# Kernel optimization log

Hardware: AMD Instinct MI355X
Metric: run time of the kernel (lower is better)

The kernel has to match this reference:

```python
import math
import jax, jax.numpy as jnp
import numpy as np

HEAD_SIZE = 64
DEPTH = 0

def lambda_init_fn(depth):
    depth = depth + 1
    return 0.8 - 0.6 * math.exp(-0.3 * depth)

def setup_inputs() -> dict:
    key = jax.random.key(0)
    ks = jax.random.split(key, 9)
    B, T, C = 4, 4096, 1024
    H2 = 2 * HEAD_SIZE  # 128
    return {
        "x":  jax.random.normal(ks[0], (B, T, C), dtype=jnp.float32),
        "Wq": jax.random.normal(ks[1], (C, H2), dtype=jnp.float32) * (C ** -0.5),
        "Wk": jax.random.normal(ks[2], (C, H2), dtype=jnp.float32) * (C ** -0.5),
        "Wv": jax.random.normal(ks[3], (C, H2), dtype=jnp.float32) * (C ** -0.5),
        "lambda_q1": jax.random.normal(ks[4], (HEAD_SIZE,), dtype=jnp.float32) * 0.1,
        "lambda_q2": jax.random.normal(ks[5], (HEAD_SIZE,), dtype=jnp.float32) * 0.1,
        "lambda_k1": jax.random.normal(ks[6], (HEAD_SIZE,), dtype=jnp.float32) * 0.1,
        "lambda_k2": jax.random.normal(ks[7], (HEAD_SIZE,), dtype=jnp.float32) * 0.1,
    }

def reference(x, Wq, Wk, Wv, lambda_q1, lambda_q2, lambda_k1, lambda_k2):
    B, T, C = x.shape
    q = x @ Wq  # (B,T,2*hs)
    k = x @ Wk
    v = x @ Wv  # (B,T,2*hs)
    q1, q2 = jnp.split(q, 2, axis=-1)
    k1, k2 = jnp.split(k, 2, axis=-1)
    scale = 1.0 / math.sqrt(HEAD_SIZE)
    w1 = jnp.einsum('btd,bsd->bts', q1, k1) * scale  # (B,T,T)
    w2 = jnp.einsum('btd,bsd->bts', q2, k2) * scale
    causal = jnp.tril(jnp.ones((T, T), dtype=bool))
    neg_inf = jnp.float32(-jnp.inf)
    w1 = jnp.where(causal, w1, neg_inf)
    w2 = jnp.where(causal, w2, neg_inf)
    lam1 = jnp.exp(jnp.sum(lambda_q1 * lambda_k1))
    lam2 = jnp.exp(jnp.sum(lambda_q2 * lambda_k2))
    lam = lam1 - lam2 + lambda_init_fn(DEPTH)
    weights = jax.nn.softmax(w1, axis=-1) - lam * jax.nn.softmax(w2, axis=-1)
    out = jnp.einsum('bts,bsd->btd', weights, v)  # (B,T,2*hs)
    return out
```

## Files before the change

### kernel.cpp

```cpp
#include <hip/hip_runtime.h>
#include <hip/hip_bf16.h>

typedef __bf16 bf16x8 __attribute__((ext_vector_type(8)));
typedef float f32x4 __attribute__((ext_vector_type(4)));

#define LAMBDA_INIT 0.3555090675909693f
#define CEXP 0.18033688011112042f

#define K_OFF   ((size_t)16384 * 128)
#define VT_OFF  ((size_t)2 * 16384 * 128)
#define PART_OFF_BYTES ((size_t)12582912)
#define REC_FLOATS 4160

__device__ __forceinline__ unsigned short f2bf(float f) {
    __hip_bfloat16 h = __float2bfloat16(f);
    unsigned short u;
    __builtin_memcpy(&u, &h, 2);
    return u;
}
__device__ __forceinline__ float bf2f(unsigned short u) {
    unsigned int x = ((unsigned int)u) << 16;
    float f;
    __builtin_memcpy(&f, &x, 4);
    return f;
}
__device__ __forceinline__ unsigned int cvt_pk_bf16(float a, float b) {
    unsigned int r;
    asm volatile("v_cvt_pk_bf16_f32 %0, %1, %2" : "=v"(r) : "v"(a), "v"(b));
    return r;
}

__global__ __launch_bounds__(256) void prep_wt(
    const float* __restrict__ Wq, const float* __restrict__ Wk,
    const float* __restrict__ Wv, unsigned short* __restrict__ WT) {
    const int kt = blockIdx.x, nt = blockIdx.y, mat = blockIdx.z;
    const float* W = (mat == 0) ? Wq : (mat == 1) ? Wk : Wv;
    unsigned short* O = WT + (size_t)mat * 128 * 1024;
    __shared__ float tb[64][65];
    const int r = threadIdx.x >> 2, c4 = (threadIdx.x & 3) * 16;
    for (int j = 0; j < 4; ++j) {
        float4 v = *(const float4*)&W[(size_t)(kt * 64 + r) * 128 + nt * 64 + c4 + j * 4];
        tb[r][c4 + j * 4 + 0] = v.x;
        tb[r][c4 + j * 4 + 1] = v.y;
        tb[r][c4 + j * 4 + 2] = v.z;
        tb[r][c4 + j * 4 + 3] = v.w;
    }
    __syncthreads();
    unsigned short tmp[16];
    for (int j = 0; j < 16; ++j) tmp[j] = f2bf(tb[c4 + j][r]);
    *(uint4*)&O[(size_t)(nt * 64 + r) * 1024 + kt * 64 + c4] = *(uint4*)&tmp[0];
    *(uint4*)&O[(size_t)(nt * 64 + r) * 1024 + kt * 64 + c4 + 8] = *(uint4*)&tmp[8];
}

__global__ __launch_bounds__(512) void qkv_fused(
    const float* __restrict__ x, const unsigned short* __restrict__ WT,
    unsigned short* __restrict__ qkv) {
    const int tid = threadIdx.x;
    const int l = tid & 63, w = tid >> 6;
    const int g = l >> 4, i16 = l & 15;
    const int rh = w >> 2, cp = w & 3;
    const int row0 = blockIdx.x * 64;
    const int np = blockIdx.y;
    const unsigned short* Wt = WT + (size_t)np * 192 * 1024;

    __shared__ unsigned short xs[64][72];
    __shared__ unsigned short wt[192][72];

    f32x4 acc[2][3];
    const f32x4 z4 = {0.f, 0.f, 0.f, 0.f};
    for (int rt = 0; rt < 2; ++rt)
        for (int ct = 0; ct < 3; ++ct) acc[rt][ct] = z4;

    const int xrow = tid >> 3, xcol = (tid & 7) * 8;
    const int wn = tid >> 3, wk8 = (tid & 7) * 8;
    const float* xp = &x[(size_t)(row0 + xrow) * 1024 + xcol];
    const unsigned short* wp = &Wt[(size_t)wn * 1024 + wk8];

    float4 ax0, ax1;
    uint4 aw0, aw1, aw2;

#define QI(k0_) do {                                                        \
        ax0 = *(const float4*)&xp[(k0_)];                                   \
        ax1 = *(const float4*)&xp[(k0_) + 4];                               \
        aw0 = *(const uint4*)&wp[(k0_)];                                    \
        aw1 = *(const uint4*)&wp[64 * 1024 + (k0_)];                        \
        aw2 = *(const uint4*)&wp[128 * 1024 + (k0_)];                       \
    } while (0)

#define QS() do {                                                           \
        *(ushort4*)&xs[xrow][xcol]     = make_ushort4(f2bf(ax0.x), f2bf(ax0.y), f2bf(ax0.z), f2bf(ax0.w)); \
        *(ushort4*)&xs[xrow][xcol + 4] = make_ushort4(f2bf(ax1.x), f2bf(ax1.y), f2bf(ax1.z), f2bf(ax1.w)); \
        *(uint4*)&wt[wn +   0][wk8] = aw0;                                  \
        *(uint4*)&wt[wn +  64][wk8] = aw1;                                  \
        *(uint4*)&wt[wn + 128][wk8] = aw2;                                  \
    } while (0)

    QI(0);
    #pragma unroll 1
    for (int k0 = 0; k0 < 1024; k0 += 64) {
        __syncthreads();
        QS();
        if (k0 + 64 < 1024) QI(k0 + 64);
        __syncthreads();
        bf16x8 af[2][2];
        #pragma unroll
        for (int rt = 0; rt < 2; ++rt)
            for (int cc = 0; cc < 2; ++cc)
                af[rt][cc] = *(const bf16x8*)&xs[rh * 32 + rt * 16 + i16][cc * 32 + 8 * g];
        #pragma unroll
        for (int ct = 0; ct < 3; ++ct)
            for (int cc = 0; cc < 2; ++cc) {
                bf16x8 bb = *(const bf16x8*)&wt[cp * 48 + ct * 16 + i16][cc * 32 + 8 * g];
                for (int rt = 0; rt < 2; ++rt)
                    acc[rt][ct] = __builtin_amdgcn_mfma_f32_16x16x32_bf16(af[rt][cc], bb, acc[rt][ct], 0, 0, 0);
            }
    }
#undef QI
#undef QS

    __syncthreads();
    unsigned short(*ts)[200] = (unsigned short(*)[200]) & wt[0][0];
    #pragma unroll
    for (int rt = 0; rt < 2; ++rt)
        for (int ct = 0; ct < 3; ++ct) {
            const float sc = (np == 0 && cp * 48 + ct * 16 < 128) ? CEXP : 1.0f;
            for (int r = 0; r < 4; ++r)
                ts[rh * 32 + rt * 16 + g * 4 + r][cp * 48 + ct * 16 + i16] = f2bf(acc[rt][ct][r] * sc);
        }
    __syncthreads();

    const int bq = row0 >> 12;
    const int s = (row0 >> 6) & 63;
    if (np == 0) {
        {
            unsigned short* outp = qkv + (size_t)row0 * 128;
            #pragma unroll
            for (int it = 0; it < 2; ++it) {
                int tr = it * 32 + (tid >> 4), dv0 = (tid & 15) * 8;
                *(uint4*)&outp[tr * 128 + dv0] = *(const uint4*)&ts[tr][dv0];
            }
        }
        {
            unsigned short* kimg = qkv + K_OFF + ((size_t)(bq * 64 + s) * 2) * 4096;
            int region = tid >> 6, slot = tid & 63;
            int row = (region >> 1) * 16 + (slot & 15);
            int d = 128 + (region & 1) * 32 + (slot >> 4) * 8;
            uint4 vv = *(const uint4*)&ts[row][d];
            *(uint4*)&kimg[(region * 64 + slot) * 8] = vv;
        }
    } else {
        {
            unsigned short* kimg = qkv + K_OFF + ((size_t)(bq * 64 + s) * 2 + 1) * 4096;
            int region = tid >> 6, slot = tid & 63;
            int row = (region >> 1) * 16 + (slot & 15);
            int d = (region & 1) * 32 + (slot >> 4) * 8;
            uint4 vv = *(const uint4*)&ts[row][d];
            *(uint4*)&kimg[(region * 64 + slot) * 8] = vv;
        }
        {
            unsigned short* vimg = qkv + VT_OFF + (size_t)(bq * 64 + s) * 8192;
            #pragma unroll
            for (int it = 0; it < 2; ++it) {
                int lin = it * 512 + tid;
                int region = lin >> 6, slot = lin & 63;
                int dv = 64 + (region >> 1) * 16 + (slot & 15);
                int kv0 = (region & 1) * 32 + (slot >> 4) * 8;
                unsigned short tmp[8];
                #pragma unroll
                for (int e = 0; e < 8; ++e) tmp[e] = ts[kv0 + e][dv];
                *(uint4*)&vimg[(region * 64 + slot) * 8] = *(uint4*)tmp;
            }
        }
    }
}

__global__ __launch_bounds__(256, 3) void diff_attn_pair(
    const unsigned short* __restrict__ q, const unsigned short* __restrict__ kimg,
    const unsigned short* __restrict__ vimg,
    float* __restrict__ part, int ncs) {
    const int bx = blockIdx.x, b = blockIdx.y;
    const int c = blockIdx.z >> 1, branch = blockIdx.z & 1;
    const int bxe = (c & 1) ? (31 - bx) : bx;
    const int t_o = 63 - 2 * bxe, t_e = t_o - 1;
    const int n = t_o + 1;
    const int s_lo = (c * n) >> ncs, smax = ((c + 1) * n) >> ncs;

    if (s_lo >= smax) return;

    const int tid = threadIdx.x;
    const int l = tid & 63, w = tid >> 6;
    const int gq = l >> 4, i16 = l & 15;
    const float NEGINF = -__builtin_inff();

    __shared__ unsigned short ksf[2][4096];
    __shared__ unsigned short psf[2][8192];

    float* recA = part + ((((size_t)(b * 64 + t_e) << ncs) + c) * 2 + branch) * REC_FLOATS;
    float* recB = part + ((((size_t)(b * 64 + t_o) << ncs) + c) * 2 + branch) * REC_FLOATS;
    const bool emptyA = (s_lo > t_e);

    const size_t bbase = (size_t)b * 4096;
    const unsigned short* kimg_b = kimg + (size_t)b * 524288;
    const unsigned short* vimg_b = vimg + (size_t)b * 524288;
    const int tid8 = tid * 8;
    const int l8 = l * 8;
    const f32x4 z4 = {0.f, 0.f, 0.f, 0.f};

    bf16x8 qfA[2], qfB[2];
    #pragma unroll
    for (int cc = 0; cc < 2; ++cc) {
        qfA[cc] = *(const bf16x8*)&q[(bbase + t_e * 64 + w * 16 + i16) * 128 + branch * 64 + cc * 32 + 8 * gq];
        qfB[cc] = *(const bf16x8*)&q[(bbase + t_o * 64 + w * 16 + i16) * 128 + branch * 64 + cc * 32 + 8 * gq];
    }

    float lsumA = 0.f, lsumB = 0.f;
    f32x4 acc[2][4][2];
    for (int qs = 0; qs < 2; ++qs)
        for (int qg = 0; qg < 4; ++qg)
            for (int j = 0; j < 2; ++j) acc[qs][qg][j] = z4;

    int pdst[4];
    #pragma unroll
    for (int cb = 0; cb < 4; ++cb)
        pdst[cb] = ((w * 2 + (cb >> 1)) * 64 + ((cb & 1) * 2 + (gq >> 1)) * 16 + i16) * 8 + (gq & 1) * 4;

    uint4 kr0, kr1;
    bf16x8 vb00, vb01, vb10, vb11;

#define K_ISSUE(s_) do {                                                            \
        const unsigned short* kp = &kimg_b[((size_t)(s_) * 2 + branch) * 4096];     \
        kr0 = *(const uint4*)&kp[tid8];                                             \
        kr1 = *(const uint4*)&kp[tid8 + 2048];                                      \
    } while (0)
#define V_ISSUE(s_) do {                                                            \
        const unsigned short* vp = &vimg_b[(size_t)(s_) * 8192 + w * 2048];         \
        vb00 = *(const bf16x8*)&vp[l8];                                             \
        vb01 = *(const bf16x8*)&vp[512 + l8];                                       \
        vb10 = *(const bf16x8*)&vp[1024 + l8];                                      \
        vb11 = *(const bf16x8*)&vp[1536 + l8];                                      \
    } while (0)

#define PV_CLUSTER(pp_, aPrev_) do {                                                \
        if (aPrev_) {                                                               \
            _Pragma("unroll")                                                       \
            for (int qg = 0; qg < 4; ++qg) {                                        \
                bf16x8 pa0 = *(const bf16x8*)&psf[pp_][(qg * 2 + 0) * 512 + l8];    \
                bf16x8 pa1 = *(const bf16x8*)&psf[pp_][(qg * 2 + 1) * 512 + l8];    \
                acc[0][qg][0] = __builtin_amdgcn_mfma_f32_16x16x32_bf16(pa0, vb00, acc[0][qg][0], 0, 0, 0); \
                acc[0][qg][0] = __builtin_amdgcn_mfma_f32_16x16x32_bf16(pa1, vb01, acc[0][qg][0], 0, 0, 0); \
                acc[0][qg][1] = __builtin_amdgcn_mfma_f32_16x16x32_bf16(pa0, vb10, acc[0][qg][1], 0, 0, 0); \
                acc[0][qg][1] = __builtin_amdgcn_mfma_f32_16x16x32_bf16(pa1, vb11, acc[0][qg][1], 0, 0, 0); \
            }                                                                       \
        }                                                                           \
        _Pragma("unroll")                                                           \
        for (int qg = 0; qg < 4; ++qg) {                                            \
            bf16x8 pa0 = *(const bf16x8*)&psf[pp_][4096 + (qg * 2 + 0) * 512 + l8]; \
            bf16x8 pa1 = *(const bf16x8*)&psf[pp_][4096 + (qg * 2 + 1) * 512 + l8]; \
            acc[1][qg][0] = __builtin_amdgcn_mfma_f32_16x16x32_bf16(pa0, vb00, acc[1][qg][0], 0, 0, 0); \
            acc[1][qg][0] = __builtin_amdgcn_mfma_f32_16x16x32_bf16(pa1, vb01, acc[1][qg][0], 0, 0, 0); \
            acc[1][qg][1] = __builtin_amdgcn_mfma_f32_16x16x32_bf16(pa0, vb10, acc[1][qg][1], 0, 0, 0); \
            acc[1][qg][1] = __builtin_amdgcn_mfma_f32_16x16x32_bf16(pa1, vb11, acc[1][qg][1], 0, 0, 0); \
        }                                                                           \
    } while (0)

    K_ISSUE(s_lo);
    #pragma unroll 1
    for (int s = s_lo; s < smax; ++s) {
        const int kb = s & 1;
        *(uint4*)&ksf[kb][tid8] = kr0;
        *(uint4*)&ksf[kb][tid8 + 2048] = kr1;
        if (s + 1 < smax) K_ISSUE(s + 1);
        __syncthreads();

        __builtin_amdgcn_s_setprio(1);
        if (s > s_lo) PV_CLUSTER((s - 1) & 1, (s - 1) != t_o);
        f32x4 scA[4], scB[4];
        for (int cb = 0; cb < 4; ++cb) { scA[cb] = z4; scB[cb] = z4; }
        #pragma unroll
        for (int cb = 0; cb < 4; ++cb)
            for (int cc = 0; cc < 2; ++cc) {
                bf16x8 kf = *(const bf16x8*)&ksf[kb][((cb * 2 + cc) * 64 + l) * 8];
                scA[cb] = __builtin_amdgcn_mfma_f32_16x16x32_bf16(kf, qfA[cc], scA[cb], 0, 0, 0);
                scB[cb] = __builtin_amdgcn_mfma_f32_16x16x32_bf16(kf, qfB[cc], scB[cb], 0, 0, 0);
            }
        __builtin_amdgcn_s_setprio(0);
        V_ISSUE(s);

        const bool aAct = (s != t_o);
        if (aAct) {
            if (s == t_e) {
                int ql = w * 16 + i16;
                for (int cb = 0; cb < 4; ++cb)
                    for (int r = 0; r < 4; ++r)
                        if (cb * 16 + gq * 4 + r > ql) scA[cb][r] = NEGINF;
            }
            #pragma unroll
            for (int cb = 0; cb < 4; ++cb) {
                float p0 = exp2f(scA[cb][0]);
                float p1 = exp2f(scA[cb][1]);
                float p2 = exp2f(scA[cb][2]);
                float p3 = exp2f(scA[cb][3]);
                lsumA += (p0 + p1) + (p2 + p3);
                uint2 pw;
                pw.x = cvt_pk_bf16(p0, p1);
                pw.y = cvt_pk_bf16(p2, p3);
                *(uint2*)&psf[kb][pdst[cb]] = pw;
            }
        }
        {
            if (s == t_o) {
                int ql = w * 16 + i16;
                for (int cb = 0; cb < 4; ++cb)
                    for (int r = 0; r < 4; ++r)
                        if (cb * 16 + gq * 4 + r > ql) scB[cb][r] = NEGINF;
            }
            #pragma unroll
            for (int cb = 0; cb < 4; ++cb) {
                float p0 = exp2f(scB[cb][0]);
                float p1 = exp2f(scB[cb][1]);
                float p2 = exp2f(scB[cb][2]);
                float p3 = exp2f(scB[cb][3]);
                lsumB += (p0 + p1) + (p2 + p3);
                uint2 pw;
                pw.x = cvt_pk_bf16(p0, p1);
                pw.y = cvt_pk_bf16(p2, p3);
                *(uint2*)&psf[kb][4096 + pdst[cb]] = pw;
            }
        }
    }

    __syncthreads();
    __builtin_amdgcn_s_setprio(1);
    PV_CLUSTER((smax - 1) & 1, (smax - 1) != t_o);
    __builtin_amdgcn_s_setprio(0);
#undef K_ISSUE
#undef V_ISSUE
#undef PV_CLUSTER

    lsumA += __shfl_xor(lsumA, 16);
    lsumA += __shfl_xor(lsumA, 32);
    lsumB += __shfl_xor(lsumB, 16);
    lsumB += __shfl_xor(lsumB, 32);
    if (!emptyA) {
        if (gq == 0) recA[w * 16 + i16] = lsumA;
        unsigned short* OA = (unsigned short*)(recA + 64);
        for (int qg = 0; qg < 4; ++qg)
            for (int j = 0; j < 2; ++j)
                for (int r = 0; r < 4; ++r)
                    OA[(qg * 16 + gq * 4 + r) * 128 + (w * 2 + j) * 16 + i16] = f2bf(acc[0][qg][j][r]);
    }
    {
        if (gq == 0) recB[w * 16 + i16] = lsumB;
        unsigned short* OB = (unsigned short*)(recB + 64);
        for (int qg = 0; qg < 4; ++qg)
            for (int j = 0; j < 2; ++j)
                for (int r = 0; r < 4; ++r)
                    OB[(qg * 16 + gq * 4 + r) * 128 + (w * 2 + j) * 16 + i16] = f2bf(acc[1][qg][j][r]);
    }
}

__global__ __launch_bounds__(256) void diff_combine(
    const float* __restrict__ part,
    const float* __restrict__ lq1, const float* __restrict__ lq2,
    const float* __restrict__ lk1, const float* __restrict__ lk2,
    float* __restrict__ out, int ncs) {
    const int t = blockIdx.x, b = blockIdx.y;
    const int tid = threadIdx.x;
    const int nc = 1 << ncs;
    const int n = (t | 1) + 1;
    __shared__ float sl[2][64];
    __shared__ float s_lam;

    const float* recbase = part + (((size_t)(b * 64 + t) << ncs)) * 2 * REC_FLOATS;

    if (tid < 64) {
        float s1 = lq1[tid] * lk1[tid];
        float s2 = lq2[tid] * lk2[tid];
        for (int off = 32; off > 0; off >>= 1) {
            s1 += __shfl_xor(s1, off);
            s2 += __shfl_xor(s2, off);
        }
        if (tid == 0) s_lam = expf(s1) - expf(s2) + LAMBDA_INIT;
    }
    if (tid < 128) {
        int r = tid & 63, br = tid >> 6;
        float acc = 0.f;
        for (int c = 0; c < nc; ++c) {
            int lo = (c * n) >> ncs, hi = ((c + 1) * n) >> ncs;
            if (lo >= hi || lo > t) continue;
            acc += recbase[(c * 2 + br) * REC_FLOATS + r];
        }
        sl[br][r] = acc;
    }
    __syncthreads();
    const float lam = s_lam;

    float* op = out + ((size_t)b * 4096 + (size_t)t * 64) * 128;
    for (int grp = 0; grp < 4; ++grp) {
        int gid = grp * 256 + tid;
        int e = gid * 8;
        int row = e >> 7;
        float o1[8] = {0, 0, 0, 0, 0, 0, 0, 0}, o2[8] = {0, 0, 0, 0, 0, 0, 0, 0};
        for (int c = 0; c < nc; ++c) {
            int lo = (c * n) >> ncs, hi = ((c + 1) * n) >> ncs;
            if (lo >= hi || lo > t) continue;
            const unsigned short* O0 = (const unsigned short*)(recbase + (c * 2 + 0) * REC_FLOATS + 64);
            const unsigned short* O1 = (const unsigned short*)(recbase + (c * 2 + 1) * REC_FLOATS + 64);
            uint4 u0 = *(const uint4*)&O0[e];
            uint4 u1 = *(const uint4*)&O1[e];
            const unsigned short* e0 = (const unsigned short*)&u0;
            const unsigned short* e1 = (const unsigned short*)&u1;
            #pragma unroll
            for (int j = 0; j < 8; ++j) {
                o1[j] += bf2f(e0[j]);
                o2[j] += bf2f(e1[j]);
            }
        }
        float l1inv = 1.0f / sl[0][row], l2inv = 1.0f / sl[1][row];
        float res[8];
        #pragma unroll
        for (int j = 0; j < 8; ++j) res[j] = o1[j] * l1inv - lam * o2[j] * l2inv;
        *(float4*)&op[e] = *(float4*)&res[0];
        *(float4*)&op[e + 4] = *(float4*)&res[4];
    }
}

extern "C" void kernel_launch(void* const* d_in, const int* in_sizes, int n_in,
                              void* d_out, int out_size, void* d_ws, size_t ws_size,
                              hipStream_t stream) {
    const float* x   = (const float*)d_in[0];
    const float* Wq  = (const float*)d_in[1];
    const float* Wk  = (const float*)d_in[2];
    const float* Wv  = (const float*)d_in[3];
    const float* lq1 = (const float*)d_in[4];
    const float* lq2 = (const float*)d_in[5];
    const float* lk1 = (const float*)d_in[6];
    const float* lk2 = (const float*)d_in[7];
    float* out = (float*)d_out;
    unsigned short* qkv = (unsigned short*)d_ws;

    const int ncs = 2;
    const size_t part_bytes = (size_t)256 * (1 << ncs) * 2 * REC_FLOATS * 4;
    float* part = (float*)((char*)d_ws + PART_OFF_BYTES);
    unsigned short* WT = (unsigned short*)((char*)d_ws + PART_OFF_BYTES + part_bytes);

    prep_wt<<<dim3(16, 2, 3), 256, 0, stream>>>(Wq, Wk, Wv, WT);
    qkv_fused<<<dim3(256, 2), 512, 0, stream>>>(x, WT, qkv);

    const unsigned short* qb = qkv;
    const unsigned short* kb = qkv + K_OFF;
    const unsigned short* vtb = qkv + VT_OFF;
    diff_attn_pair<<<dim3(32, 4, 2 << ncs), 256, 0, stream>>>(qb, kb, vtb, part, ncs);
    diff_combine<<<dim3(64, 4), 256, 0, stream>>>(part, lq1, lq2, lk1, lk2, out, ncs);
}
```

Baseline: 91.84 us.

## Split KV range into fixed-size chunks and simplify PV pipeline for occupancy

Replaces the proportional 4-way split of each query pair's key range with fixed chunks of 8 or 16 key blocks, picked by available workspace. Empty chunks exit early, giving many more uniformly sized blocks. The PV product moves from the next iteration into the current one after a barrier. That drops the double-buffered P tile, shrinks LDS and allows a launch bound of 5 waves. The cost is an extra barrier per iteration, less overlap of V loads with compute, and more partial records for the combine kernel to reduce.

```diff
diff --git a/kernel.cpp b/kernel.cpp
--- a/kernel.cpp
+++ b/kernel.cpp
@@ -174,18 +174,18 @@
     }
 }
 
-__global__ __launch_bounds__(256, 3) void diff_attn_pair(
+__global__ __launch_bounds__(256, 5) void diff_attn_pair(
     const unsigned short* __restrict__ q, const unsigned short* __restrict__ kimg,
     const unsigned short* __restrict__ vimg,
-    float* __restrict__ part, int ncs) {
+    float* __restrict__ part, int chs) {
     const int bx = blockIdx.x, b = blockIdx.y;
     const int c = blockIdx.z >> 1, branch = blockIdx.z & 1;
     const int bxe = (c & 1) ? (31 - bx) : bx;
     const int t_o = 63 - 2 * bxe, t_e = t_o - 1;
     const int n = t_o + 1;
-    const int s_lo = (c * n) >> ncs, smax = ((c + 1) * n) >> ncs;
-
-    if (s_lo >= smax) return;
+    const int s_lo = c << chs;
+    if (s_lo >= n) return;
+    const int smax = min(n, s_lo + (1 << chs));
 
     const int tid = threadIdx.x;
     const int l = tid & 63, w = tid >> 6;
@@ -193,10 +193,11 @@
     const float NEGINF = -__builtin_inff();
 
     __shared__ unsigned short ksf[2][4096];
-    __shared__ unsigned short psf[2][8192];
-
-    float* recA = part + ((((size_t)(b * 64 + t_e) << ncs) + c) * 2 + branch) * REC_FLOATS;
-    float* recB = part + ((((size_t)(b * 64 + t_o) << ncs) + c) * 2 + branch) * REC_FLOATS;
+    __shared__ unsigned short psf[8192];
+
+    const int rshift = 6 - chs;
+    float* recA = part + ((((size_t)(b * 64 + t_e) << rshift) + c) * 2 + branch) * REC_FLOATS;
+    float* recB = part + ((((size_t)(b * 64 + t_o) << rshift) + c) * 2 + branch) * REC_FLOATS;
     const bool emptyA = (s_lo > t_e);
 
     const size_t bbase = (size_t)b * 4096;
@@ -240,53 +241,29 @@
         vb11 = *(const bf16x8*)&vp[1536 + l8];                                      \
     } while (0)
 
-#define PV_CLUSTER(pp_, aPrev_) do {                                                \
-        if (aPrev_) {                                                               \
-            _Pragma("unroll")                                                       \
-            for (int qg = 0; qg < 4; ++qg) {                                        \
-                bf16x8 pa0 = *(const bf16x8*)&psf[pp_][(qg * 2 + 0) * 512 + l8];    \
-                bf16x8 pa1 = *(const bf16x8*)&psf[pp_][(qg * 2 + 1) * 512 + l8];    \
-                acc[0][qg][0] = __builtin_amdgcn_mfma_f32_16x16x32_bf16(pa0, vb00, acc[0][qg][0], 0, 0, 0); \
-                acc[0][qg][0] = __builtin_amdgcn_mfma_f32_16x16x32_bf16(pa1, vb01, acc[0][qg][0], 0, 0, 0); \
-                acc[0][qg][1] = __builtin_amdgcn_mfma_f32_16x16x32_bf16(pa0, vb10, acc[0][qg][1], 0, 0, 0); \
-                acc[0][qg][1] = __builtin_amdgcn_mfma_f32_16x16x32_bf16(pa1, vb11, acc[0][qg][1], 0, 0, 0); \
-            }                                                                       \
-        }                                                                           \
-        _Pragma("unroll")                                                           \
-        for (int qg = 0; qg < 4; ++qg) {                                            \
-            bf16x8 pa0 = *(const bf16x8*)&psf[pp_][4096 + (qg * 2 + 0) * 512 + l8]; \
-            bf16x8 pa1 = *(const bf16x8*)&psf[pp_][4096 + (qg * 2 + 1) * 512 + l8]; \
-            acc[1][qg][0] = __builtin_amdgcn_mfma_f32_16x16x32_bf16(pa0, vb00, acc[1][qg][0], 0, 0, 0); \
-            acc[1][qg][0] = __builtin_amdgcn_mfma_f32_16x16x32_bf16(pa1, vb01, acc[1][qg][0], 0, 0, 0); \
-            acc[1][qg][1] = __builtin_amdgcn_mfma_f32_16x16x32_bf16(pa0, vb10, acc[1][qg][1], 0, 0, 0); \
-            acc[1][qg][1] = __builtin_amdgcn_mfma_f32_16x16x32_bf16(pa1, vb11, acc[1][qg][1], 0, 0, 0); \
-        }                                                                           \
-    } while (0)
-
     K_ISSUE(s_lo);
+    V_ISSUE(s_lo);
+    int pb = 0;
     #pragma unroll 1
     for (int s = s_lo; s < smax; ++s) {
-        const int kb = s & 1;
-        *(uint4*)&ksf[kb][tid8] = kr0;
-        *(uint4*)&ksf[kb][tid8 + 2048] = kr1;
+        *(uint4*)&ksf[pb][tid8] = kr0;
+        *(uint4*)&ksf[pb][tid8 + 2048] = kr1;
         if (s + 1 < smax) K_ISSUE(s + 1);
         __syncthreads();
-
-        __builtin_amdgcn_s_setprio(1);
-        if (s > s_lo) PV_CLUSTER((s - 1) & 1, (s - 1) != t_o);
+        const bool aAct = (s != t_o);
+
         f32x4 scA[4], scB[4];
         for (int cb = 0; cb < 4; ++cb) { scA[cb] = z4; scB[cb] = z4; }
+        __builtin_amdgcn_s_setprio(1);
         #pragma unroll
         for (int cb = 0; cb < 4; ++cb)
             for (int cc = 0; cc < 2; ++cc) {
-                bf16x8 kf = *(const bf16x8*)&ksf[kb][((cb * 2 + cc) * 64 + l) * 8];
+                bf16x8 kf = *(const bf16x8*)&ksf[pb][((cb * 2 + cc) * 64 + l) * 8];
                 scA[cb] = __builtin_amdgcn_mfma_f32_16x16x32_bf16(kf, qfA[cc], scA[cb], 0, 0, 0);
                 scB[cb] = __builtin_amdgcn_mfma_f32_16x16x32_bf16(kf, qfB[cc], scB[cb], 0, 0, 0);
             }
         __builtin_amdgcn_s_setprio(0);
-        V_ISSUE(s);
-
-        const bool aAct = (s != t_o);
+
         if (aAct) {
             if (s == t_e) {
                 int ql = w * 16 + i16;
@@ -304,7 +281,7 @@
                 uint2 pw;
                 pw.x = cvt_pk_bf16(p0, p1);
                 pw.y = cvt_pk_bf16(p2, p3);
-                *(uint2*)&psf[kb][pdst[cb]] = pw;
+                *(uint2*)&psf[pdst[cb]] = pw;
             }
         }
         {
@@ -324,18 +301,38 @@
                 uint2 pw;
                 pw.x = cvt_pk_bf16(p0, p1);
                 pw.y = cvt_pk_bf16(p2, p3);
-                *(uint2*)&psf[kb][4096 + pdst[cb]] = pw;
-            }
-        }
-    }
-
-    __syncthreads();
-    __builtin_amdgcn_s_setprio(1);
-    PV_CLUSTER((smax - 1) & 1, (smax - 1) != t_o);
-    __builtin_amdgcn_s_setprio(0);
+                *(uint2*)&psf[4096 + pdst[cb]] = pw;
+            }
+        }
+        __syncthreads();
+
+        __builtin_amdgcn_s_setprio(1);
+        if (aAct) {
+            #pragma unroll
+            for (int qg = 0; qg < 4; ++qg) {
+                bf16x8 pa0 = *(const bf16x8*)&psf[(qg * 2 + 0) * 512 + l8];
+                bf16x8 pa1 = *(const bf16x8*)&psf[(qg * 2 + 1) * 512 + l8];
+                acc[0][qg][0] = __builtin_amdgcn_mfma_f32_16x16x32_bf16(pa0, vb00, acc[0][qg][0], 0, 0, 0);
+                acc[0][qg][0] = __builtin_amdgcn_mfma_f32_16x16x32_bf16(pa1, vb01, acc[0][qg][0], 0, 0, 0);
+                acc[0][qg][1] = __builtin_amdgcn_mfma_f32_16x16x32_bf16(pa0, vb10, acc[0][qg][1], 0, 0, 0);
+                acc[0][qg][1] = __builtin_amdgcn_mfma_f32_16x16x32_bf16(pa1, vb11, acc[0][qg][1], 0, 0, 0);
+            }
+        }
+        #pragma unroll
+        for (int qg = 0; qg < 4; ++qg) {
+            bf16x8 pa0 = *(const bf16x8*)&psf[4096 + (qg * 2 + 0) * 512 + l8];
+            bf16x8 pa1 = *(const bf16x8*)&psf[4096 + (qg * 2 + 1) * 512 + l8];
+            acc[1][qg][0] = __builtin_amdgcn_mfma_f32_16x16x32_bf16(pa0, vb00, acc[1][qg][0], 0, 0, 0);
+            acc[1][qg][0] = __builtin_amdgcn_mfma_f32_16x16x32_bf16(pa1, vb01, acc[1][qg][0], 0, 0, 0);
+            acc[1][qg][1] = __builtin_amdgcn_mfma_f32_16x16x32_bf16(pa0, vb10, acc[1][qg][1], 0, 0, 0);
+            acc[1][qg][1] = __builtin_amdgcn_mfma_f32_16x16x32_bf16(pa1, vb11, acc[1][qg][1], 0, 0, 0);
+        }
+        __builtin_amdgcn_s_setprio(0);
+        if (s + 1 < smax) V_ISSUE(s + 1);
+        pb ^= 1;
+    }
 #undef K_ISSUE
 #undef V_ISSUE
-#undef PV_CLUSTER
 
     lsumA += __shfl_xor(lsumA, 16);
     lsumA += __shfl_xor(lsumA, 32);
@@ -363,15 +360,15 @@
     const float* __restrict__ part,
     const float* __restrict__ lq1, const float* __restrict__ lq2,
     const float* __restrict__ lk1, const float* __restrict__ lk2,
-    float* __restrict__ out, int ncs) {
+    float* __restrict__ out, int chs) {
     const int t = blockIdx.x, b = blockIdx.y;
     const int tid = threadIdx.x;
-    const int nc = 1 << ncs;
-    const int n = (t | 1) + 1;
+    const int nc = 64 >> chs;
+    const int rshift = 6 - chs;
     __shared__ float sl[2][64];
     __shared__ float s_lam;
 
-    const float* recbase = part + (((size_t)(b * 64 + t) << ncs)) * 2 * REC_FLOATS;
+    const float* recbase = part + ((size_t)(b * 64 + t) << rshift) * 2 * REC_FLOATS;
 
     if (tid < 64) {
         float s1 = lq1[tid] * lk1[tid];
@@ -386,8 +383,7 @@
         int r = tid & 63, br = tid >> 6;
         float acc = 0.f;
         for (int c = 0; c < nc; ++c) {
-            int lo = (c * n) >> ncs, hi = ((c + 1) * n) >> ncs;
-            if (lo >= hi || lo > t) continue;
+            if ((c << chs) > t) break;
             acc += recbase[(c * 2 + br) * REC_FLOATS + r];
         }
         sl[br][r] = acc;
@@ -402,8 +398,7 @@
         int row = e >> 7;
         float o1[8] = {0, 0, 0, 0, 0, 0, 0, 0}, o2[8] = {0, 0, 0, 0, 0, 0, 0, 0};
         for (int c = 0; c < nc; ++c) {
-            int lo = (c * n) >> ncs, hi = ((c + 1) * n) >> ncs;
-            if (lo >= hi || lo > t) continue;
+            if ((c << chs) > t) break;
             const unsigned short* O0 = (const unsigned short*)(recbase + (c * 2 + 0) * REC_FLOATS + 64);
             const unsigned short* O1 = (const unsigned short*)(recbase + (c * 2 + 1) * REC_FLOATS + 64);
             uint4 u0 = *(const uint4*)&O0[e];
@@ -439,8 +434,13 @@
     float* out = (float*)d_out;
     unsigned short* qkv = (unsigned short*)d_ws;
 
-    const int ncs = 2;
-    const size_t part_bytes = (size_t)256 * (1 << ncs) * 2 * REC_FLOATS * 4;
+    const size_t WT_BYTES = (size_t)384 * 1024 * 2;
+    int chs = 4;
+    {
+        size_t part8 = (size_t)256 * 8 * 2 * REC_FLOATS * 4;
+        if (ws_size >= PART_OFF_BYTES + part8 + WT_BYTES) chs = 3;
+    }
+    const size_t part_bytes = (size_t)256 * (64 >> chs) * 2 * REC_FLOATS * 4;
     float* part = (float*)((char*)d_ws + PART_OFF_BYTES);
     unsigned short* WT = (unsigned short*)((char*)d_ws + PART_OFF_BYTES + part_bytes);
 
@@ -450,6 +450,6 @@
     const unsigned short* qb = qkv;
     const unsigned short* kb = qkv + K_OFF;
     const unsigned short* vtb = qkv + VT_OFF;
-    diff_attn_pair<<<dim3(32, 4, 2 << ncs), 256, 0, stream>>>(qb, kb, vtb, part, ncs);
-    diff_combine<<<dim3(64, 4), 256, 0, stream>>>(part, lq1, lq2, lk1, lk2, out, ncs);
-}
+    diff_attn_pair<<<dim3(32, 4, 2 * (64 >> chs)), 256, 0, stream>>>(qb, kb, vtb, part, chs);
+    diff_combine<<<dim3(64, 4), 256, 0, stream>>>(part, lq1, lq2, lk1, lk2, out, chs);
+}
```

New measurement: 260.5 us. +183.6%, slower.
